# Kernel tuning notes

Measured on AMD Instinct MI355X. Metric: run time of the kernel, lower is better.

The kernel has to match this reference:

```python
import jax, jax.numpy as jnp
import numpy as np

NH = 16   # num heads
CS = 16   # inner chunk size

def _gelu(x):
    return jax.nn.gelu(x, approximate=True)

def _diff_gelu(x):
    t = jnp.tanh(0.79788456 * x * (1.0 + 0.044715 * x * x))
    return 0.5 * x * ((1.0 - t * t) * (0.79788456 + 0.1070322243 * x * x)) + 0.5 * (1.0 + t)

def _ln_fused_l2_bwd(x, tgt, gamma, beta, eps=1e-6):
    # x, tgt: [B*nh, CS, f]; gamma/beta: [1, nh, 1, f]
    Bnh, N, HF = x.shape
    mu = x.mean(-1, keepdims=True)
    var = x.var(-1, keepdims=True)
    std = jnp.sqrt(var + eps)
    x_hat = (x - mu) / std
    y = gamma * x_hat.reshape(-1, NH, N, HF) + beta
    go = y - tgt.reshape(-1, NH, N, HF)
    gxh = (go * gamma).reshape(Bnh, N, HF)
    return (HF * gxh - gxh.sum(-1, keepdims=True) - x_hat * (gxh * x_hat).sum(-1, keepdims=True)) / (HF * std)

def setup_inputs() -> dict:
    key = jax.random.key(0)
    ks = jax.random.split(key, 8)
    B, nh, f, hf4, n_chunks = 4, NH, 64, 256, 128
    Bnh = B * nh
    XQ = jax.random.normal(ks[0], (n_chunks, Bnh, CS, f), jnp.float32)
    XK = jax.random.normal(ks[1], (n_chunks, Bnh, CS, f), jnp.float32)
    XV = jax.random.normal(ks[2], (n_chunks, Bnh, CS, f), jnp.float32)
    # inner-loop lr coeffs (ilr * token_idx ~ lr/head_dim): small positive
    coeff = jax.random.uniform(ks[3], (n_chunks, Bnh, CS, 1), jnp.float32) * 0.01
    coeff_last = jax.random.uniform(ks[4], (n_chunks, Bnh, 1, 1), jnp.float32) * 0.01
    W1 = jax.random.normal(ks[5], (Bnh, f, hf4), jnp.float32) * 0.02
    b1 = jnp.zeros((Bnh, 1, hf4), jnp.float32)
    W2 = jax.random.normal(ks[6], (Bnh, hf4, f), jnp.float32) * 0.02
    b2 = jnp.zeros((Bnh, 1, f), jnp.float32)
    ln_weight = jnp.ones((1, nh, 1, f), jnp.float32)
    ln_bias = jnp.zeros((1, nh, 1, f), jnp.float32)
    return dict(XQ=XQ, XK=XK, XV=XV, coeff=coeff, coeff_last=coeff_last,
                W1=W1, b1=b1, W2=W2, b2=b2, ln_weight=ln_weight, ln_bias=ln_bias)

def reference(XQ, XK, XV, coeff, coeff_last, W1, b1, W2, b2, ln_weight, ln_bias):
    n_chunks, Bnh, _, f = XQ.shape
    attn_b = jnp.tril(jnp.ones((CS, CS), XQ.dtype))

    def step(carry, inp):
        W1c, b1c, W2c, b2c = carry
        xv, xk, xq, c, cl = inp
        Z1 = xk @ W1c + b1c                      # [Bnh, CS, 4f]
        X2 = _gelu(Z1)
        Z2 = X2 @ W2c + b2c                      # [Bnh, CS, f]
        dZ2 = _ln_fused_l2_bwd(Z2, xv - xk, ln_weight, ln_bias)
        dZ1 = (dZ2 @ W2c.transpose(0, 2, 1)) * _diff_gelu(Z1)
        b1_bar = b1c - c * (attn_b @ dZ1)
        A1 = jnp.tril(xq @ xk.transpose(0, 2, 1))
        Z1_bar = xq @ W1c - c * (A1 @ dZ1) + b1_bar
        X2_bar = _gelu(Z1_bar)
        b2_bar = b2c - c * (attn_b @ dZ2)
        A2 = jnp.tril(X2_bar @ X2.transpose(0, 2, 1))
        Z2_bar = X2_bar @ W2c - c * (A2 @ dZ2) + b2_bar
        W1n = W1c - cl * (xk.transpose(0, 2, 1) @ dZ1)
        W2n = W2c - cl * (X2.transpose(0, 2, 1) @ dZ2)
        return (W1n, b1_bar[:, -1:], W2n, b2_bar[:, -1:]), Z2_bar

    _, Z2_all = jax.lax.scan(step, (W1, b1, W2, b2), (XV, XK, XQ, coeff, coeff_last))
    # [n_chunks, Bnh, CS, f] -> [Bnh, N, f]
    return Z2_all.transpose(1, 0, 2, 3).reshape(Bnh, n_chunks * CS, f)
```

## Files before the change

kernel.cpp:

```cpp
#include <hip/hip_runtime.h>

typedef __attribute__((ext_vector_type(8))) short bf16x8;
typedef __attribute__((ext_vector_type(4))) float f32x4;
typedef __attribute__((ext_vector_type(2))) unsigned int u32x2;
typedef __attribute__((ext_vector_type(4))) unsigned int u32x4;

#define MFMA16(a,b,c) __builtin_amdgcn_mfma_f32_16x16x32_bf16(a,b,c,0,0,0)
#define A_GELU 0.7978845608028654f

#define OFF_W1B   0u
#define OFF_W2F   36864u
#define OFF_W2T   70656u
#define OFF_XK    107520u
#define OFF_XQ    109824u
#define OFF_XKT   112128u
#define OFF_X2    115200u
#define OFF_X2B   123648u
#define OFF_DZ2B  132096u
#define OFF_DZ1CT 134400u
#define OFF_DZ2CT 146688u
#define OFF_M1    149760u
#define OFF_M2    150528u
#define OFF_Z2F   151296u
#define OFF_Z2G   155520u
#define OFF_TGT   159744u
#define OFF_B2    162048u
#define OFF_COEF  162560u
#define OFF_CL    162624u
#define SMEM_BYTES 162640u

__device__ __forceinline__ float fast_tanh(float u){
    float e = __expf(2.0f*u);
    return 1.0f - 2.0f/(e + 1.0f);
}
__device__ __forceinline__ float gelu_f(float x){
    float t = fast_tanh(A_GELU*(x + 0.044715f*x*x*x));
    return 0.5f*x*(1.0f+t);
}
__device__ __forceinline__ float dgelu_f(float x){
    float x2 = x*x;
    float t = fast_tanh(A_GELU*x*(1.0f + 0.044715f*x2));
    return 0.5f*x*((1.0f-t*t)*(A_GELU + 0.1070322243f*x2)) + 0.5f*(1.0f+t);
}
__device__ __forceinline__ short f2bf(float f){
    unsigned u = __builtin_bit_cast(unsigned, f);
    u += 0x7FFFu + ((u >> 16) & 1u);
    return (short)(u >> 16);
}
__device__ __forceinline__ float bf2f(unsigned short s){
    unsigned u = ((unsigned)s) << 16;
    return __builtin_bit_cast(float, u);
}
__device__ __forceinline__ unsigned pkbf(float a, float b){
    unsigned r;
    asm("v_cvt_pk_bf16_f32 %0, %1, %2" : "=v"(r) : "v"(a), "v"(b));
    return r;
}
__device__ __forceinline__ bf16x8 ldfrag(const unsigned short* p){
    return *(const bf16x8*)p;
}
__device__ __forceinline__ bf16x8 ldmask16(const unsigned short* row, int hi){
    bf16x8 r = {0,0,0,0,0,0,0,0};
    if (hi < 2) r = *(const bf16x8*)(row + hi*8);
    return r;
}

__global__ __launch_bounds__(512, 1)
void ttt_m2(const float* __restrict__ XQ, const float* __restrict__ XK,
            const float* __restrict__ XV, const float* __restrict__ coeff,
            const float* __restrict__ coeff_last,
            const float* __restrict__ W1g, const float* __restrict__ b1g,
            const float* __restrict__ W2g, const float* __restrict__ b2g,
            const float* __restrict__ gammag, const float* __restrict__ betag,
            float* __restrict__ out)
{
    const int h  = blockIdx.x;
    const int t  = threadIdx.x;
    const int l  = t & 63;
    const int w  = t >> 6;
    const int lo = l & 15;
    const int hi = l >> 4;

    extern __shared__ char smem[];
    unsigned short* sW1bu  = (unsigned short*)(smem + OFF_W1B);
    unsigned short* sW2fu  = (unsigned short*)(smem + OFF_W2F);
    unsigned short* sW2T   = (unsigned short*)(smem + OFF_W2T);
    unsigned short* sxku   = (unsigned short*)(smem + OFF_XK);
    unsigned short* sxqu   = (unsigned short*)(smem + OFF_XQ);
    unsigned short* sxkT   = (unsigned short*)(smem + OFF_XKT);
    unsigned short* sX2u   = (unsigned short*)(smem + OFF_X2);
    unsigned short* sX2bu  = (unsigned short*)(smem + OFF_X2B);
    unsigned short* sdZ2bu = (unsigned short*)(smem + OFF_DZ2B);
    unsigned short* sdZ1ct = (unsigned short*)(smem + OFF_DZ1CT);
    unsigned short* sdZ2ct = (unsigned short*)(smem + OFF_DZ2CT);
    unsigned short* sM1u   = (unsigned short*)(smem + OFF_M1);
    unsigned short* sM2u   = (unsigned short*)(smem + OFF_M2);
    float* sZ2f  = (float*)(smem + OFF_Z2F);
    float* sZ2g  = (float*)(smem + OFF_Z2G);
    unsigned short* stgtu = (unsigned short*)(smem + OFF_TGT);
    float* b2f   = (float*)(smem + OFF_B2);
    float* scoef = (float*)(smem + OFF_COEF);
    float* sCL   = (float*)(smem + OFF_CL);

    const int base1 = h*16384;
    const int base2 = h*16384;

    float mW1[4][2][4];
    float mW2T[4][2][4];
    #pragma unroll
    for (int mt = 0; mt < 4; ++mt)
      #pragma unroll
      for (int tix = 0; tix < 2; ++tix)
        #pragma unroll
        for (int reg = 0; reg < 4; ++reg) {
            const int m = mt*16 + hi*4 + reg, n = (2*w + tix)*16 + lo;
            mW1[mt][tix][reg] = W1g[base1 + m*256 + n];
        }
    #pragma unroll
    for (int ft = 0; ft < 4; ++ft)
      #pragma unroll
      for (int tix = 0; tix < 2; ++tix)
        #pragma unroll
        for (int reg = 0; reg < 4; ++reg) {
            const int f = ft*16 + hi*4 + reg, hf = (2*w + tix)*16 + lo;
            mW2T[ft][tix][reg] = W2g[base2 + hf*64 + f];
        }
    float b1reg[2];
    b1reg[0] = b1g[h*256 + (2*w)*16 + lo];
    b1reg[1] = b1g[h*256 + (2*w+1)*16 + lo];

    for (int i = 0; i < 32; ++i) {
        const int idx = i*512 + t;
        const int m = idx >> 8, n = idx & 255;
        sW1bu[n*72 + m] = f2bf(W1g[base1 + idx]);
    }
    for (int i = 0; i < 32; ++i) {
        const int idx = i*512 + t;
        const int hf = idx >> 6, f = idx & 63;
        const short v = f2bf(W2g[base2 + idx]);
        sW2fu[f*264 + hf] = v;
        sW2T[hf*72 + f]   = v;
    }
    if (t < 64) b2f[t] = b2g[h*64 + t];

    const float gj = gammag[(h & 15)*64 + l];
    const float bj = betag [(h & 15)*64 + l];

    {
        const int r0 = w*2;
        const float xk0 = XK[h*1024 + r0*64 + l],     xq0 = XQ[h*1024 + r0*64 + l];
        const float xk1 = XK[h*1024 + (r0+1)*64 + l], xq1 = XQ[h*1024 + (r0+1)*64 + l];
        const float xv0 = XV[h*1024 + r0*64 + l],     xv1 = XV[h*1024 + (r0+1)*64 + l];
        const unsigned pkk = pkbf(xk0, xk1), pkq = pkbf(xq0, xq1);
        const unsigned pkt = pkbf(xv0 - xk0, xv1 - xk1);
        sxku[r0*72 + l]     = (unsigned short)pkk;
        sxku[(r0+1)*72 + l] = (unsigned short)(pkk >> 16);
        sxqu[r0*72 + l]     = (unsigned short)pkq;
        sxqu[(r0+1)*72 + l] = (unsigned short)(pkq >> 16);
        *(unsigned*)&sxkT[l*24 + r0] = pkk;
        stgtu[r0*72 + l]     = (unsigned short)pkt;
        stgtu[(r0+1)*72 + l] = (unsigned short)(pkt >> 16);
        if (t < 16)  scoef[t] = coeff[h*16 + t];
        if (t == 16) sCL[0]   = coeff_last[h];
    }
    __syncthreads();

    bf16x8 w1f[2][2];
    #pragma unroll
    for (int tix = 0; tix < 2; ++tix) {
        const int n = (2*w + tix)*16 + lo;
        w1f[tix][0] = ldfrag(sW1bu + n*72 + hi*8);
        w1f[tix][1] = ldfrag(sW1bu + n*72 + 32 + hi*8);
    }

    for (int ci = 0; ci < 128; ++ci) {
        const float clv = sCL[0];
        const float c15 = scoef[15];
        float crs[4];
        #pragma unroll
        for (int reg = 0; reg < 4; ++reg) crs[reg] = scoef[hi*4 + reg];

        float pxk[4], pxq[4], pxv[4];
        float pcf = 0.f, pcl = 0.f;
        if (w >= 4 && ci < 127) {
            const int cb1 = (ci + 1)*65536 + h*1024;
            const int r0 = (w - 4)*4;
            #pragma unroll
            for (int i = 0; i < 4; ++i) {
                pxk[i] = XK[cb1 + (r0 + i)*64 + l];
                pxq[i] = XQ[cb1 + (r0 + i)*64 + l];
                pxv[i] = XV[cb1 + (r0 + i)*64 + l];
            }
            const int u = t - 256;
            if (u < 16)  pcf = coeff[(ci + 1)*1024 + h*16 + u];
            if (u == 16) pcl = coeff_last[(ci + 1)*64 + h];
        }

        float z1s[8];
        unsigned px2[2][2];
        bf16x8 afk0 = ldfrag(sxku + lo*72 + hi*8);
        bf16x8 afk1 = ldfrag(sxku + lo*72 + 32 + hi*8);
        #pragma unroll
        for (int tix = 0; tix < 2; ++tix) {
            const int n = (2*w + tix)*16 + lo;
            f32x4 acc = {b1reg[tix], b1reg[tix], b1reg[tix], b1reg[tix]};
            acc = MFMA16(afk0, w1f[tix][0], acc);
            acc = MFMA16(afk1, w1f[tix][1], acc);
            float g[4];
            #pragma unroll
            for (int reg = 0; reg < 4; ++reg) {
                z1s[tix*4 + reg] = acc[reg];
                g[reg] = gelu_f(acc[reg]);
            }
            const unsigned p01 = pkbf(g[0], g[1]), p23 = pkbf(g[2], g[3]);
            px2[tix][0] = p01; px2[tix][1] = p23;
            sX2u[(hi*4+0)*264 + n] = (unsigned short)p01;
            sX2u[(hi*4+1)*264 + n] = (unsigned short)(p01 >> 16);
            sX2u[(hi*4+2)*264 + n] = (unsigned short)p23;
            sX2u[(hi*4+3)*264 + n] = (unsigned short)(p23 >> 16);
        }
        if (w == 0) {
            bf16x8 aq0 = ldfrag(sxqu + lo*72 + hi*8);
            bf16x8 aq1 = ldfrag(sxqu + lo*72 + 32 + hi*8);
            f32x4 a1 = {0.f, 0.f, 0.f, 0.f};
            a1 = MFMA16(aq0, afk0, a1);
            a1 = MFMA16(aq1, afk1, a1);
            #pragma unroll
            for (int reg = 0; reg < 4; ++reg) {
                const int r = hi*4 + reg;
                const float v = (lo <= r) ? (-crs[reg]*(a1[reg] + 1.0f)) : 0.0f;
                sM1u[r*24 + lo] = f2bf(v);
            }
        }
        #pragma unroll
        for (int ft = 0; ft < 4; ++ft)
          #pragma unroll
          for (int tix = 0; tix < 2; ++tix) {
                const int hf = (2*w + tix)*16 + lo, f0 = ft*16 + hi*4;
                const unsigned p01 = pkbf(mW2T[ft][tix][0], mW2T[ft][tix][1]);
                const unsigned p23 = pkbf(mW2T[ft][tix][2], mW2T[ft][tix][3]);
                *(u32x2*)&sW2T[hf*72 + f0] = (u32x2){p01, p23};
                sW2fu[(f0+0)*264 + hf] = (unsigned short)p01;
                sW2fu[(f0+1)*264 + hf] = (unsigned short)(p01 >> 16);
                sW2fu[(f0+2)*264 + hf] = (unsigned short)p23;
                sW2fu[(f0+3)*264 + hf] = (unsigned short)(p23 >> 16);
          }
        __syncthreads();

        const int tile = w & 3, kh = w >> 2;
        const int nf = tile*16 + lo;
        {
            f32x4 acc;
            if (kh == 0) {
                const float b2v = b2f[(ci & 1)*64 + nf];
                acc = (f32x4){b2v, b2v, b2v, b2v};
            } else acc = (f32x4){0.f, 0.f, 0.f, 0.f};
            #pragma unroll
            for (int s = 0; s < 4; ++s) {
                const int k = (kh*4 + s)*32 + hi*8;
                acc = MFMA16(ldfrag(sX2u + lo*264 + k),
                             ldfrag(sW2fu + nf*264 + k), acc);
            }
            float* dst = (kh == 0) ? sZ2g : sZ2f;
            #pragma unroll
            for (int reg = 0; reg < 4; ++reg)
                dst[(hi*4 + reg)*66 + nf] = acc[reg];
        }
        __syncthreads();

        {
            float dzp[2];
            #pragma unroll
            for (int i = 0; i < 2; ++i) {
                const int r = w*2 + i;
                const float z2 = sZ2f[r*66 + l] + sZ2g[r*66 + l];
                float s1 = z2, s2 = z2*z2;
                #pragma unroll
                for (int m = 1; m < 64; m <<= 1) { s1 += __shfl_xor(s1, m); s2 += __shfl_xor(s2, m); }
                const float mu   = s1*(1.0f/64.0f);
                const float var  = s2*(1.0f/64.0f) - mu*mu;
                const float rstd = rsqrtf(var + 1e-6f);
                const float xh   = (z2 - mu)*rstd;
                const float go   = gj*xh + bj - bf2f(stgtu[r*72 + l]);
                const float gg   = go*gj;
                float u1 = gg, u2 = gg*xh;
                #pragma unroll
                for (int m = 1; m < 64; m <<= 1) { u1 += __shfl_xor(u1, m); u2 += __shfl_xor(u2, m); }
                dzp[i] = (64.0f*gg - u1 - xh*u2)*(rstd*(1.0f/64.0f));
            }
            const unsigned pk = pkbf(dzp[0], dzp[1]);
            sdZ2bu[(w*2)*72 + l]   = (unsigned short)pk;
            sdZ2bu[(w*2+1)*72 + l] = (unsigned short)(pk >> 16);
            *(unsigned*)&sdZ2ct[l*24 + w*2] = pk;
        }
        __syncthreads();

        {
            bf16x8 ad0 = ldfrag(sdZ2bu + lo*72 + hi*8);
            bf16x8 ad1 = ldfrag(sdZ2bu + lo*72 + 32 + hi*8);
            float b1old[2];
            #pragma unroll
            for (int tix = 0; tix < 2; ++tix) {
                const int n = (2*w + tix)*16 + lo;
                f32x4 acc = {0.f, 0.f, 0.f, 0.f};
                acc = MFMA16(ad0, ldfrag(sW2T + n*72 + hi*8), acc);
                acc = MFMA16(ad1, ldfrag(sW2T + n*72 + 32 + hi*8), acc);
                float dv[4], cs = 0.f;
                #pragma unroll
                for (int reg = 0; reg < 4; ++reg) {
                    dv[reg] = acc[reg]*dgelu_f(z1s[tix*4 + reg]);
                    cs += dv[reg];
                }
                *(u32x2*)&sdZ1ct[n*24 + hi*4] =
                    (u32x2){pkbf(dv[0], dv[1]), pkbf(dv[2], dv[3])};
                cs += __shfl_xor(cs, 16);
                cs += __shfl_xor(cs, 32);
                b1old[tix] = b1reg[tix];
                b1reg[tix] -= c15*cs;
            }
            bf16x8 aq0 = ldfrag(sxqu + lo*72 + hi*8);
            bf16x8 aq1 = ldfrag(sxqu + lo*72 + 32 + hi*8);
            bf16x8 am1 = ldmask16(sM1u + lo*24, hi);
            #pragma unroll
            for (int tix = 0; tix < 2; ++tix) {
                const int n = (2*w + tix)*16 + lo;
                f32x4 acc = {b1old[tix], b1old[tix], b1old[tix], b1old[tix]};
                acc = MFMA16(aq0, w1f[tix][0], acc);
                acc = MFMA16(aq1, w1f[tix][1], acc);
                acc = MFMA16(am1, ldmask16(sdZ1ct + n*24, hi), acc);
                float g[4];
                #pragma unroll
                for (int reg = 0; reg < 4; ++reg) g[reg] = gelu_f(acc[reg]);
                const unsigned p01 = pkbf(g[0], g[1]), p23 = pkbf(g[2], g[3]);
                sX2bu[(hi*4+0)*264 + n] = (unsigned short)p01;
                sX2bu[(hi*4+1)*264 + n] = (unsigned short)(p01 >> 16);
                sX2bu[(hi*4+2)*264 + n] = (unsigned short)p23;
                sX2bu[(hi*4+3)*264 + n] = (unsigned short)(p23 >> 16);
            }
            bf16x8 bz0 = ldmask16(sdZ1ct + ((2*w)*16 + lo)*24, hi);
            bf16x8 bz1 = ldmask16(sdZ1ct + ((2*w+1)*16 + lo)*24, hi);
            #pragma unroll
            for (int mt = 0; mt < 4; ++mt) {
                bf16x8 axt = ldmask16(sxkT + (mt*16 + lo)*24, hi);
                f32x4 z4 = {0.f,0.f,0.f,0.f};
                f32x4 u0 = MFMA16(axt, bz0, z4);
                f32x4 u1 = MFMA16(axt, bz1, z4);
                #pragma unroll
                for (int reg = 0; reg < 4; ++reg) {
                    mW1[mt][0][reg] -= clv*u0[reg];
                    mW1[mt][1][reg] -= clv*u1[reg];
                }
            }
        }
        __syncthreads();

        {
            bf16x8 bz2[4];
            #pragma unroll
            for (int nt = 0; nt < 4; ++nt)
                bz2[nt] = ldmask16(sdZ2ct + (nt*16 + lo)*24, hi);
            bf16x8 xf[2];
            {
                const int base = lo + 32*(hi & 1);
                #pragma unroll
                for (int tix = 0; tix < 2; ++tix) {
                    unsigned w0 = (unsigned)__shfl((int)px2[tix][0], base);
                    unsigned w1 = (unsigned)__shfl((int)px2[tix][1], base);
                    unsigned w2 = (unsigned)__shfl((int)px2[tix][0], base + 16);
                    unsigned w3 = (unsigned)__shfl((int)px2[tix][1], base + 16);
                    if (hi >= 2) { w0 = 0; w1 = 0; w2 = 0; w3 = 0; }
                    xf[tix] = __builtin_bit_cast(bf16x8, (u32x4){w0, w1, w2, w3});
                }
            }
            #pragma unroll
            for (int ft = 0; ft < 4; ++ft)
                #pragma unroll
                for (int tix = 0; tix < 2; ++tix) {
                    f32x4 z4 = {0.f,0.f,0.f,0.f};
                    f32x4 u = MFMA16(bz2[ft], xf[tix], z4);
                    #pragma unroll
                    for (int reg = 0; reg < 4; ++reg)
                        mW2T[ft][tix][reg] -= clv*u[reg];
                }
            if (w == 0) {
                f32x4 a2 = {0.f,0.f,0.f,0.f};
                #pragma unroll
                for (int ks = 0; ks < 8; ++ks) {
                    const int k = ks*32 + hi*8;
                    a2 = MFMA16(ldfrag(sX2bu + lo*264 + k),
                                ldfrag(sX2u + lo*264 + k), a2);
                }
                #pragma unroll
                for (int reg = 0; reg < 4; ++reg) {
                    const int r = hi*4 + reg;
                    const float v = (lo <= r) ? (-crs[reg]*(a2[reg] + 1.0f)) : 0.0f;
                    sM2u[r*24 + lo] = f2bf(v);
                }
            }
            if (w == 1) {
                bf16x8 c0 = ldfrag(sdZ2ct + l*24);
                bf16x8 c1 = ldfrag(sdZ2ct + l*24 + 8);
                float cs = 0.f;
                #pragma unroll
                for (int j = 0; j < 8; ++j)
                    cs += bf2f((unsigned short)c0[j]) + bf2f((unsigned short)c1[j]);
                b2f[((ci + 1) & 1)*64 + l] = b2f[(ci & 1)*64 + l] - c15*cs;
            }
            #pragma unroll
            for (int mt = 0; mt < 4; ++mt)
              #pragma unroll
              for (int tix = 0; tix < 2; ++tix) {
                    const int n = (2*w + tix)*16 + lo, m0 = mt*16 + hi*4;
                    *(u32x2*)&sW1bu[n*72 + m0] =
                        (u32x2){pkbf(mW1[mt][tix][0], mW1[mt][tix][1]),
                                pkbf(mW1[mt][tix][2], mW1[mt][tix][3])};
              }
        }
        __syncthreads();

        #pragma unroll
        for (int tix = 0; tix < 2; ++tix) {
            const int n = (2*w + tix)*16 + lo;
            w1f[tix][0] = ldfrag(sW1bu + n*72 + hi*8);
            w1f[tix][1] = ldfrag(sW1bu + n*72 + 32 + hi*8);
        }
        if (w < 4) {
            const int nf2 = w*16 + lo;
            const float b2v = b2f[(ci & 1)*64 + nf2];
            f32x4 acc = {b2v, b2v, b2v, b2v};
            #pragma unroll
            for (int s = 0; s < 8; ++s) {
                const int k0 = s*32 + hi*8;
                acc = MFMA16(ldfrag(sX2bu + lo*264 + k0),
                             ldfrag(sW2fu + nf2*264 + k0), acc);
            }
            acc = MFMA16(ldmask16(sM2u + lo*24, hi),
                         ldmask16(sdZ2ct + nf2*24, hi), acc);
            #pragma unroll
            for (int reg = 0; reg < 4; ++reg)
                out[h*131072 + (ci*16 + hi*4 + reg)*64 + nf2] = acc[reg];
        } else if (ci < 127) {
            const int r0 = (w - 4)*4;
            #pragma unroll
            for (int p = 0; p < 2; ++p) {
                const int r = r0 + 2*p;
                const unsigned pkk = pkbf(pxk[2*p], pxk[2*p+1]);
                const unsigned pkq = pkbf(pxq[2*p], pxq[2*p+1]);
                const unsigned pkt = pkbf(pxv[2*p] - pxk[2*p], pxv[2*p+1] - pxk[2*p+1]);
                sxku[r*72 + l]     = (unsigned short)pkk;
                sxku[(r+1)*72 + l] = (unsigned short)(pkk >> 16);
                sxqu[r*72 + l]     = (unsigned short)pkq;
                sxqu[(r+1)*72 + l] = (unsigned short)(pkq >> 16);
                *(unsigned*)&sxkT[l*24 + r] = pkk;
                stgtu[r*72 + l]     = (unsigned short)pkt;
                stgtu[(r+1)*72 + l] = (unsigned short)(pkt >> 16);
            }
            const int u = t - 256;
            if (u < 16)  scoef[u] = pcf;
            if (u == 16) sCL[0]   = pcl;
        }
        __syncthreads();
    }
}

extern "C" void kernel_launch(void* const* d_in, const int* in_sizes, int n_in,
                              void* d_out, int out_size, void* d_ws, size_t ws_size,
                              hipStream_t stream) {
    const float* XQ  = (const float*)d_in[0];
    const float* XK  = (const float*)d_in[1];
    const float* XV  = (const float*)d_in[2];
    const float* cf  = (const float*)d_in[3];
    const float* cfl = (const float*)d_in[4];
    const float* W1  = (const float*)d_in[5];
    const float* b1  = (const float*)d_in[6];
    const float* W2  = (const float*)d_in[7];
    const float* b2  = (const float*)d_in[8];
    const float* gam = (const float*)d_in[9];
    const float* bet = (const float*)d_in[10];
    float* o = (float*)d_out;

    hipFuncSetAttribute((const void*)ttt_m2,
                        hipFuncAttributeMaxDynamicSharedMemorySize, SMEM_BYTES);
    ttt_m2<<<64, 512, SMEM_BYTES, stream>>>(XQ, XK, XV, cf, cfl, W1, b1, W2, b2, gam, bet, o);
}
```

Measured before the change: 860.0 us.

## Swizzle X2/W2 shared-memory layouts and use DPP wave reductions for layernorm

Applies an XOR swizzle on the hidden-dimension index for the sX2, sX2b and sW2f shared buffers, on both the write side and the MFMA fragment-read side, to cut LDS bank conflicts. It also replaces the 6-step shfl_xor butterfly reductions in the layernorm backward with DPP row operations followed by two cross-row shuffles. The swizzle must match exactly between every writer and reader of these buffers, otherwise results will be wrong.

```diff
diff --git a/kernel.cpp b/kernel.cpp
--- a/kernel.cpp
+++ b/kernel.cpp
@@ -64,6 +64,21 @@
     if (hi < 2) r = *(const bf16x8*)(row + hi*8);
     return r;
 }
+template<int CTRL>
+__device__ __forceinline__ float dppadd(float v){
+    int y = __builtin_amdgcn_update_dpp(0, __builtin_bit_cast(int, v),
+                                        CTRL, 0xF, 0xF, true);
+    return v + __builtin_bit_cast(float, y);
+}
+__device__ __forceinline__ float wsum(float v){
+    v = dppadd<0xB1>(v);
+    v = dppadd<0x4E>(v);
+    v = dppadd<0x141>(v);
+    v = dppadd<0x140>(v);
+    v += __shfl_xor(v, 16);
+    v += __shfl_xor(v, 32);
+    return v;
+}
 
 __global__ __launch_bounds__(512, 1)
 void ttt_m2(const float* __restrict__ XQ, const float* __restrict__ XK,
@@ -80,6 +95,9 @@
     const int w  = t >> 6;
     const int lo = l & 15;
     const int hi = l >> 4;
+
+    const int w2k = (hi >> 1) << 4;
+    const int rdk = (lo & 8) << 1;
 
     extern __shared__ char smem[];
     unsigned short* sW1bu  = (unsigned short*)(smem + OFF_W1B);
@@ -138,8 +156,8 @@
         const int idx = i*512 + t;
         const int hf = idx >> 6, f = idx & 63;
         const short v = f2bf(W2g[base2 + idx]);
-        sW2fu[f*264 + hf] = v;
-        sW2T[hf*72 + f]   = v;
+        sW2fu[f*264 + (hf ^ ((f & 8) << 1))] = v;
+        sW2T[hf*72 + f] = v;
     }
     if (t < 64) b2f[t] = b2g[h*64 + t];
 
@@ -214,10 +232,11 @@
             }
             const unsigned p01 = pkbf(g[0], g[1]), p23 = pkbf(g[2], g[3]);
             px2[tix][0] = p01; px2[tix][1] = p23;
-            sX2u[(hi*4+0)*264 + n] = (unsigned short)p01;
-            sX2u[(hi*4+1)*264 + n] = (unsigned short)(p01 >> 16);
-            sX2u[(hi*4+2)*264 + n] = (unsigned short)p23;
-            sX2u[(hi*4+3)*264 + n] = (unsigned short)(p23 >> 16);
+            const int nsw = n ^ w2k;
+            sX2u[(hi*4+0)*264 + nsw] = (unsigned short)p01;
+            sX2u[(hi*4+1)*264 + nsw] = (unsigned short)(p01 >> 16);
+            sX2u[(hi*4+2)*264 + nsw] = (unsigned short)p23;
+            sX2u[(hi*4+3)*264 + nsw] = (unsigned short)(p23 >> 16);
         }
         if (w == 0) {
             bf16x8 aq0 = ldfrag(sxqu + lo*72 + hi*8);
@@ -240,10 +259,11 @@
                 const unsigned p01 = pkbf(mW2T[ft][tix][0], mW2T[ft][tix][1]);
                 const unsigned p23 = pkbf(mW2T[ft][tix][2], mW2T[ft][tix][3]);
                 *(u32x2*)&sW2T[hf*72 + f0] = (u32x2){p01, p23};
-                sW2fu[(f0+0)*264 + hf] = (unsigned short)p01;
-                sW2fu[(f0+1)*264 + hf] = (unsigned short)(p01 >> 16);
-                sW2fu[(f0+2)*264 + hf] = (unsigned short)p23;
-                sW2fu[(f0+3)*264 + hf] = (unsigned short)(p23 >> 16);
+                const int hfs = hf ^ w2k;
+                sW2fu[(f0+0)*264 + hfs] = (unsigned short)p01;
+                sW2fu[(f0+1)*264 + hfs] = (unsigned short)(p01 >> 16);
+                sW2fu[(f0+2)*264 + hfs] = (unsigned short)p23;
+                sW2fu[(f0+3)*264 + hfs] = (unsigned short)(p23 >> 16);
           }
         __syncthreads();
 
@@ -257,7 +277,7 @@
             } else acc = (f32x4){0.f, 0.f, 0.f, 0.f};
             #pragma unroll
             for (int s = 0; s < 4; ++s) {
-                const int k = (kh*4 + s)*32 + hi*8;
+                const int k = ((kh*4 + s)*32 + hi*8) ^ rdk;
                 acc = MFMA16(ldfrag(sX2u + lo*264 + k),
                              ldfrag(sW2fu + nf*264 + k), acc);
             }
@@ -274,18 +294,16 @@
             for (int i = 0; i < 2; ++i) {
                 const int r = w*2 + i;
                 const float z2 = sZ2f[r*66 + l] + sZ2g[r*66 + l];
-                float s1 = z2, s2 = z2*z2;
-                #pragma unroll
-                for (int m = 1; m < 64; m <<= 1) { s1 += __shfl_xor(s1, m); s2 += __shfl_xor(s2, m); }
+                const float s1 = wsum(z2);
+                const float s2 = wsum(z2*z2);
                 const float mu   = s1*(1.0f/64.0f);
                 const float var  = s2*(1.0f/64.0f) - mu*mu;
                 const float rstd = rsqrtf(var + 1e-6f);
                 const float xh   = (z2 - mu)*rstd;
                 const float go   = gj*xh + bj - bf2f(stgtu[r*72 + l]);
                 const float gg   = go*gj;
-                float u1 = gg, u2 = gg*xh;
-                #pragma unroll
-                for (int m = 1; m < 64; m <<= 1) { u1 += __shfl_xor(u1, m); u2 += __shfl_xor(u2, m); }
+                const float u1 = wsum(gg);
+                const float u2 = wsum(gg*xh);
                 dzp[i] = (64.0f*gg - u1 - xh*u2)*(rstd*(1.0f/64.0f));
             }
             const unsigned pk = pkbf(dzp[0], dzp[1]);
@@ -332,10 +350,11 @@
                 #pragma unroll
                 for (int reg = 0; reg < 4; ++reg) g[reg] = gelu_f(acc[reg]);
                 const unsigned p01 = pkbf(g[0], g[1]), p23 = pkbf(g[2], g[3]);
-                sX2bu[(hi*4+0)*264 + n] = (unsigned short)p01;
-                sX2bu[(hi*4+1)*264 + n] = (unsigned short)(p01 >> 16);
-                sX2bu[(hi*4+2)*264 + n] = (unsigned short)p23;
-                sX2bu[(hi*4+3)*264 + n] = (unsigned short)(p23 >> 16);
+                const int nsw = n ^ w2k;
+                sX2bu[(hi*4+0)*264 + nsw] = (unsigned short)p01;
+                sX2bu[(hi*4+1)*264 + nsw] = (unsigned short)(p01 >> 16);
+                sX2bu[(hi*4+2)*264 + nsw] = (unsigned short)p23;
+                sX2bu[(hi*4+3)*264 + nsw] = (unsigned short)(p23 >> 16);
             }
             bf16x8 bz0 = ldmask16(sdZ1ct + ((2*w)*16 + lo)*24, hi);
             bf16x8 bz1 = ldmask16(sdZ1ct + ((2*w+1)*16 + lo)*24, hi);
@@ -386,7 +405,7 @@
                 f32x4 a2 = {0.f,0.f,0.f,0.f};
                 #pragma unroll
                 for (int ks = 0; ks < 8; ++ks) {
-                    const int k = ks*32 + hi*8;
+                    const int k = (ks*32 + hi*8) ^ rdk;
                     a2 = MFMA16(ldfrag(sX2bu + lo*264 + k),
                                 ldfrag(sX2u + lo*264 + k), a2);
                 }
@@ -430,7 +449,7 @@
             f32x4 acc = {b2v, b2v, b2v, b2v};
             #pragma unroll
             for (int s = 0; s < 8; ++s) {
-                const int k0 = s*32 + hi*8;
+                const int k0 = (s*32 + hi*8) ^ rdk;
                 acc = MFMA16(ldfrag(sX2bu + lo*264 + k0),
                              ldfrag(sW2fu + nf2*264 + k0), acc);
             }
```

After: 1.072 ms. 1.25x slower.
